# Optimization experiments

Hardware: AMD Instinct MI355X
Metric: run time of the kernel (lower is better)

Reference implementation:

```python
import jax, jax.numpy as jnp
import numpy as np

LOG_ZERO = -1e30
LOG_EPS = 1e-12


def spectral_norm(W, u0, target_radius=0.99):
    """3-step power iteration (u,v detached, as in torch no_grad) then scale W to radius 0.99."""
    Ws = jax.lax.stop_gradient(W)
    u = u0 / (jnp.linalg.norm(u0) + 1e-8)
    v = None
    for _ in range(3):
        v = Ws.T @ u
        v = v / (jnp.linalg.norm(v) + 1e-8)
        u = Ws @ v
        u = u / (jnp.linalg.norm(u) + 1e-8)
    sigma = jnp.abs(u @ (W @ v))  # grads flow through W only
    return W * (target_radius / (sigma + 1e-8))


def run_cell(x, log_h0, sign_h0, R_h, R_x, R_delta, W_delta, W_out, b, b_delta, n_groups):
    T, B, D = x.shape
    G = n_groups
    gs = D // G

    def step(carry, x_t):
        lh, sh = carry
        h_prev = sh * jnp.exp(lh)  # from_log_space
        v = x_t @ R_x.T + h_prev @ R_h.T + b
        cand = jnp.tanh(v)
        delta = jax.nn.sigmoid(x_t @ W_delta.T + h_prev @ R_delta.T + b_delta)
        h_new = (1.0 - delta) * h_prev + delta * cand
        lh_new = jnp.log(jnp.abs(h_new) + LOG_EPS)  # to_log_space
        sh_new = jnp.where(h_new >= 0, 1.0, -1.0).astype(h_new.dtype)
        compete = jax.nn.softmax(h_new.reshape(B, G, gs), axis=-1).reshape(B, D)
        out = compete * jax.nn.silu(h_new @ W_out.T)
        return (lh_new, sh_new), (out, lh_new, sh_new, h_new)

    _, (out, lh_seq, sh_seq, h_lin) = jax.lax.scan(step, (log_h0, sign_h0), x)
    log_h = jnp.concatenate([log_h0[None], lh_seq], axis=0)   # [T+1,B,D]
    sign_h = jnp.concatenate([sign_h0[None], sh_seq], axis=0)  # [T+1,B,D]
    return out, log_h, sign_h, h_lin


def setup_inputs() -> dict:
    T, B, D = 1024, 8, 1024
    key = jax.random.key(0)
    ks = jax.random.split(key, 9)
    s = 1.0 / np.sqrt(D)
    xavier = np.sqrt(2.0 / (D + D))
    return {
        "x": jax.random.normal(ks[0], (T, B, D), jnp.float32),
        "log_h0": jnp.full((B, D), LOG_ZERO, jnp.float32),
        "sign_h0": jnp.ones((B, D), jnp.float32),
        "R_h_raw": jax.random.normal(ks[1], (D, D), jnp.float32) * s,
        "R_x": jax.random.normal(ks[2], (D, D), jnp.float32) * s,
        "R_delta_raw": jax.random.normal(ks[3], (D, D), jnp.float32) * s,
        "W_delta": jax.random.normal(ks[4], (D, D), jnp.float32) * (0.1 * xavier),
        "W_out": jax.random.normal(ks[5], (D, D), jnp.float32) * xavier,
        "b": jnp.zeros((D,), jnp.float32),
        "b_delta": jnp.full((D,), -2.0, jnp.float32),
        "u_h": jax.random.normal(ks[6], (D,), jnp.float32),
        "u_delta": jax.random.normal(ks[7], (D,), jnp.float32),
        "n_groups": 32,
    }


def reference(x, log_h0, sign_h0, R_h_raw, R_x, R_delta_raw, W_delta, W_out, b, b_delta, u_h, u_delta, n_groups):
    R_h = spectral_norm(R_h_raw, u_h)
    R_delta = spectral_norm(R_delta_raw, u_delta)
    return run_cell(x, log_h0, sign_h0, R_h, R_x, R_delta, W_delta, W_out, b, b_delta, n_groups)
```

## Files before the change

kernel.cpp:

```cpp
#include <hip/hip_runtime.h>
#include <hip/hip_fp16.h>

#define DD 1024
#define TSTEPS 1024
#define BATCH 8
#define NWG 64
#define ROWS 16
#define HFS 1028

typedef _Float16 half8 __attribute__((ext_vector_type(8)));
typedef float floatx4 __attribute__((ext_vector_type(4)));

#define OUT_OFF   0
#define LOGH_OFF  8388608
#define SIGNH_OFF 16785408
#define HLIN_OFF  25182208

#define WS_SCALES  0
#define WS_SUMSQ   64
#define WS_FLAGS   128
#define WS_CNTS    384
#define WS_SPECVEC 512
#define WS_COMM    16896

__device__ __forceinline__ int aload_i(int* p) { return __hip_atomic_load(p, __ATOMIC_RELAXED, __HIP_MEMORY_SCOPE_AGENT); }
__device__ __forceinline__ float aload_f(float* p) { return __hip_atomic_load(p, __ATOMIC_RELAXED, __HIP_MEMORY_SCOPE_AGENT); }
__device__ __forceinline__ unsigned aload_u(unsigned* p) { return __hip_atomic_load(p, __ATOMIC_RELAXED, __HIP_MEMORY_SCOPE_AGENT); }
__device__ __forceinline__ void astore_f(float* p, float v) { __hip_atomic_store(p, v, __ATOMIC_RELAXED, __HIP_MEMORY_SCOPE_AGENT); }
__device__ __forceinline__ void astore_i(int* p, int v) { __hip_atomic_store(p, v, __ATOMIC_RELAXED, __HIP_MEMORY_SCOPE_AGENT); }
__device__ __forceinline__ void astore_u(unsigned* p, unsigned v) { __hip_atomic_store(p, v, __ATOMIC_RELAXED, __HIP_MEMORY_SCOPE_AGENT); }
__device__ __forceinline__ void aadd_i(int* p, int v) { (void)__hip_atomic_fetch_add(p, v, __ATOMIC_RELAXED, __HIP_MEMORY_SCOPE_AGENT); }
__device__ __forceinline__ void waitcnt_vm0() { asm volatile("s_waitcnt vmcnt(0)" ::: "memory"); }

__global__ __launch_bounds__(256) void spectral_kernel(
    const float* __restrict__ Wh, const float* __restrict__ Wd,
    const float* __restrict__ uh, const float* __restrict__ ud,
    unsigned char* __restrict__ ws) {
  const int g  = blockIdx.x >> 6;
  const int wg = blockIdx.x & 63;
  const int tid = threadIdx.x;
  const float* W  = g ? Wd : Wh;
  const float* u0 = g ? ud : uh;
  float* scales = (float*)(ws + WS_SCALES);
  float* sumsq  = (float*)(ws + WS_SUMSQ) + g*8;
  int*   cnt    = (int*)(ws + WS_CNTS) + g*8;
  float* ubuf   = (float*)(ws + WS_SPECVEC) + g*2048;
  float* vbuf   = ubuf + 1024;

  __shared__ float xs[1024];
  __shared__ float tileW[256*17];
  __shared__ float red[16*17];

  float ss = 0.f;
  for (int i2 = tid; i2 < 1024; i2 += 256) { float x = u0[i2]; ss += x*x; }
  #pragma unroll
  for (int off = 1; off < 64; off <<= 1) ss += __shfl_xor(ss, off);
  if ((tid & 63) == 0) red[tid >> 6] = ss;
  __syncthreads();
  float inv_prev = 1.f/(sqrtf(red[0]+red[1]+red[2]+red[3]) + 1e-8f);
  __syncthreads();

  for (int p = 1; p <= 6; ++p) {
    const int colmv = p & 1;
    float* dst  = colmv ? vbuf : ubuf;
    float* srcw = colmv ? ubuf : vbuf;
    float part = 0.f;
    if (colmv) {
      const int jb = wg*16;
      const int jl = tid & 15, is = tid >> 4;
      float acc = 0.f;
      for (int i0 = 0; i0 < 1024; i0 += 256) {
        __syncthreads();
        float xv = (p == 1) ? u0[i0 + tid] : aload_f(srcw + i0 + tid);
        xs[tid] = xv * inv_prev;
        const float* wr = W + (size_t)(i0 + tid)*DD + jb;
        float4 a = *(const float4*)(wr + 0);
        float4 bq = *(const float4*)(wr + 4);
        float4 cq = *(const float4*)(wr + 8);
        float4 dq = *(const float4*)(wr + 12);
        float* tr = tileW + tid*17;
        tr[0]=a.x; tr[1]=a.y; tr[2]=a.z; tr[3]=a.w;
        tr[4]=bq.x; tr[5]=bq.y; tr[6]=bq.z; tr[7]=bq.w;
        tr[8]=cq.x; tr[9]=cq.y; tr[10]=cq.z; tr[11]=cq.w;
        tr[12]=dq.x; tr[13]=dq.y; tr[14]=dq.z; tr[15]=dq.w;
        __syncthreads();
        #pragma unroll 4
        for (int ii = 0; ii < 16; ++ii)
          acc += tileW[(is*16 + ii)*17 + jl] * xs[is*16 + ii];
      }
      __syncthreads();
      red[is*17 + jl] = acc;
      __syncthreads();
      if (tid < 16) {
        float y = 0.f;
        #pragma unroll
        for (int k = 0; k < 16; ++k) y += red[k*17 + tid];
        astore_f(dst + jb + tid, y);
        part = y*y;
      }
    } else {
      const int ib = wg*16;
      for (int i2 = tid; i2 < 1024; i2 += 256) xs[i2] = aload_f(srcw + i2) * inv_prev;
      __syncthreads();
      const int r = tid >> 4, s = tid & 15;
      const float* wr = W + (size_t)(ib + r)*DD;
      float acc = 0.f;
      #pragma unroll 8
      for (int jj = 0; jj < 64; ++jj) {
        int j = s + (jj << 4);
        acc += wr[j] * xs[j];
      }
      #pragma unroll
      for (int off = 1; off < 16; off <<= 1) acc += __shfl_xor(acc, off);
      __syncthreads();
      if (s == 0) red[r] = acc;
      __syncthreads();
      if (tid < 16) {
        float y = red[tid];
        astore_f(dst + ib + tid, y);
        part = y*y;
      }
    }
    #pragma unroll
    for (int off = 1; off < 16; off <<= 1) part += __shfl_xor(part, off);
    if (tid == 0) atomicAdd(sumsq + p, part);
    waitcnt_vm0();
    __syncthreads();
    if (tid == 0) {
      aadd_i(cnt + p, 1);
      while (aload_i(cnt + p) < 64) __builtin_amdgcn_s_sleep(1);
    }
    __syncthreads();
    float stot = aload_f(sumsq + p);
    inv_prev = 1.f/(sqrtf(stot) + 1e-8f);
    __syncthreads();
  }
  if (wg == 0 && tid == 0) {
    float n2 = aload_f(sumsq + 6);
    float nn = sqrtf(n2);
    float sigma = (nn*nn)/(nn + 1e-8f);
    scales[g] = 0.99f/(sigma + 1e-8f);
  }
}

__device__ __forceinline__ half8 cvt8(const float* p) {
  float4 lo = *(const float4*)p;
  float4 hi = *(const float4*)(p+4);
  half8 h;
  h[0]=(_Float16)lo.x; h[1]=(_Float16)lo.y; h[2]=(_Float16)lo.z; h[3]=(_Float16)lo.w;
  h[4]=(_Float16)hi.x; h[5]=(_Float16)hi.y; h[6]=(_Float16)hi.z; h[7]=(_Float16)hi.w;
  return h;
}

__global__ __launch_bounds__(256) void gemm_f16(
    const float* __restrict__ A,
    const float* __restrict__ B1, const float* __restrict__ B2,
    const float* __restrict__ bias1, const float* __restrict__ bias2,
    float* __restrict__ C1, float* __restrict__ C2) {
  const int n0 = blockIdx.x * 64;
  const int m0 = blockIdx.y * 64;
  const int tid = threadIdx.x;
  const int wave = tid >> 6, lane = tid & 63;
  const int quad = lane >> 4, l16 = lane & 15;
  const bool dual = (B2 != nullptr);
  __shared__ _Float16 As[64*40];
  __shared__ _Float16 Bs1[64*40];
  __shared__ _Float16 Bs2[64*40];
  floatx4 zero = {0.f,0.f,0.f,0.f};
  floatx4 acc1[2][2] = {{zero,zero},{zero,zero}};
  floatx4 acc2[2][2] = {{zero,zero},{zero,zero}};
  const int srow = tid >> 2;
  const int sseg = (tid & 3) * 8;
  const int mb = (wave >> 1)*32, nb = (wave & 1)*32;
  for (int k0 = 0; k0 < 1024; k0 += 32) {
    __syncthreads();
    *(half8*)&As[srow*40 + sseg]  = cvt8(A  + (size_t)(m0+srow)*DD + k0 + sseg);
    *(half8*)&Bs1[srow*40 + sseg] = cvt8(B1 + (size_t)(n0+srow)*DD + k0 + sseg);
    if (dual) *(half8*)&Bs2[srow*40 + sseg] = cvt8(B2 + (size_t)(n0+srow)*DD + k0 + sseg);
    __syncthreads();
    half8 a0 = *(const half8*)&As[(mb + l16)*40 + quad*8];
    half8 a1 = *(const half8*)&As[(mb + 16 + l16)*40 + quad*8];
    half8 b0 = *(const half8*)&Bs1[(nb + l16)*40 + quad*8];
    half8 b1 = *(const half8*)&Bs1[(nb + 16 + l16)*40 + quad*8];
    acc1[0][0] = __builtin_amdgcn_mfma_f32_16x16x32_f16(a0, b0, acc1[0][0], 0,0,0);
    acc1[0][1] = __builtin_amdgcn_mfma_f32_16x16x32_f16(a0, b1, acc1[0][1], 0,0,0);
    acc1[1][0] = __builtin_amdgcn_mfma_f32_16x16x32_f16(a1, b0, acc1[1][0], 0,0,0);
    acc1[1][1] = __builtin_amdgcn_mfma_f32_16x16x32_f16(a1, b1, acc1[1][1], 0,0,0);
    if (dual) {
      half8 c0 = *(const half8*)&Bs2[(nb + l16)*40 + quad*8];
      half8 c1 = *(const half8*)&Bs2[(nb + 16 + l16)*40 + quad*8];
      acc2[0][0] = __builtin_amdgcn_mfma_f32_16x16x32_f16(a0, c0, acc2[0][0], 0,0,0);
      acc2[0][1] = __builtin_amdgcn_mfma_f32_16x16x32_f16(a0, c1, acc2[0][1], 0,0,0);
      acc2[1][0] = __builtin_amdgcn_mfma_f32_16x16x32_f16(a1, c0, acc2[1][0], 0,0,0);
      acc2[1][1] = __builtin_amdgcn_mfma_f32_16x16x32_f16(a1, c1, acc2[1][1], 0,0,0);
    }
  }
  #pragma unroll
  for (int in = 0; in < 2; ++in) {
    const int n = n0 + nb + in*16 + l16;
    const float bv1 = bias1 ? bias1[n] : 0.f;
    const float bv2 = (dual && bias2) ? bias2[n] : 0.f;
    #pragma unroll
    for (int im = 0; im < 2; ++im) {
      const int mrow = m0 + mb + im*16 + quad*4;
      floatx4 c = acc1[im][in];
      #pragma unroll
      for (int r2 = 0; r2 < 4; ++r2) C1[(size_t)(mrow + r2)*DD + n] = c[r2] + bv1;
      if (dual) {
        floatx4 c2 = acc2[im][in];
        #pragma unroll
        for (int r2 = 0; r2 < 4; ++r2) C2[(size_t)(mrow + r2)*DD + n] = c2[r2] + bv2;
      }
    }
  }
}

__global__ __launch_bounds__(256, 1) void recurrence_kernel(
    const float* __restrict__ Rh_raw, const float* __restrict__ Rd_raw,
    const float* __restrict__ logh0, const float* __restrict__ signh0,
    float* __restrict__ dout, unsigned char* __restrict__ ws) {
  const int wg = blockIdx.x;
  const int i0 = wg * ROWS;
  const int tid = threadIdx.x;
  const int wave = tid >> 6, lane = tid & 63;
  const int quad = lane >> 4, l16 = lane & 15;

  float* out_ax = dout + OUT_OFF;
  float* hlin   = dout + HLIN_OFF;
  float* logh   = dout + LOGH_OFF;
  float* signh  = dout + SIGNH_OFF;
  const float* scales = (const float*)(ws + WS_SCALES);
  unsigned* comm = (unsigned*)(ws + WS_COMM);
  int* flags = (int*)(ws + WS_FLAGS);

  __shared__ _Float16 hf[16*HFS];
  __shared__ floatx4 scr_v[4][64];
  __shared__ floatx4 scr_d[4][64];
  __shared__ unsigned hs[64];

  for (int idx = tid; idx < 8*HFS; idx += 256) hf[8*HFS + idx] = (_Float16)0.f;

  const float sh = scales[0], sd = scales[1];
  half8 afv[8], afd[8];
  {
    const float* rv = Rh_raw + (size_t)(i0 + l16)*DD;
    const float* rd = Rd_raw + (size_t)(i0 + l16)*DD;
    for (int ks = 0; ks < 8; ++ks) {
      const int kb = wave*256 + ks*32 + quad*8;
      half8 hv, hd;
      #pragma unroll
      for (int j = 0; j < 8; ++j) {
        hv[j] = (_Float16)(rv[kb + j] * sh);
        hd[j] = (_Float16)(rd[kb + j] * sd);
      }
      afv[ks] = hv; afd[ks] = hd;
    }
  }

  const int em = tid & 15;
  const int eb = tid >> 4;
  const bool ep = (tid < 128);
  const int ei = i0 + em;
  float hp = 0.f;
  if (ep) hp = signh0[eb*DD + ei] * expf(logh0[eb*DD + ei]);

  __syncthreads();

  for (int t = 0; t < TSTEPS; ++t) {
    float axv = 0.f, adv = 0.f;
    if (ep) {
      axv = out_ax[(size_t)(t*8 + eb)*DD + ei];
      adv = hlin[(size_t)(t*8 + eb)*DD + ei];
    }
    float vsum = 0.f, dsum = 0.f;
    if (t > 0) {
      {
        unsigned long long mask;
        do {
          int fv = aload_i(flags + lane);
          mask = __ballot(fv >= t);
        } while (mask != ~0ull);
      }
      {
        unsigned* src = comm + ((t-1)&1)*4096;
        unsigned rbuf[16];
        #pragma unroll
        for (int q = 0; q < 16; ++q) rbuf[q] = aload_u(src + q*256 + tid);
        #pragma unroll
        for (int q = 0; q < 16; ++q) {
          const int w = q*256 + tid;
          const int b2 = w >> 9;
          const int k2 = w & 511;
          *(unsigned*)&hf[b2*HFS + k2*2] = rbuf[q];
        }
      }
      __syncthreads();
      floatx4 av = {0.f,0.f,0.f,0.f}, ad2 = {0.f,0.f,0.f,0.f};
      const int kw = wave*256;
      #pragma unroll
      for (int ks = 0; ks < 8; ++ks) {
        half8 bfrag = *(const half8*)&hf[l16*HFS + kw + ks*32 + quad*8];
        av  = __builtin_amdgcn_mfma_f32_16x16x32_f16(afv[ks], bfrag, av,  0, 0, 0);
        ad2 = __builtin_amdgcn_mfma_f32_16x16x32_f16(afd[ks], bfrag, ad2, 0, 0, 0);
      }
      scr_v[wave][lane] = av;
      scr_d[wave][lane] = ad2;
      __syncthreads();
      if (ep) {
        const int rl = ((em >> 2) << 4) + eb;
        const int rr = em & 3;
        #pragma unroll
        for (int w2 = 0; w2 < 4; ++w2) {
          vsum += scr_v[w2][rl][rr];
          dsum += scr_d[w2][rl][rr];
        }
      }
    }
    float hn = 0.f, logv = 0.f, sgn = 1.f;
    if (ep) {
      float v  = axv + vsum;
      float dd = adv + dsum;
      float cand  = tanhf(v);
      float delta = 1.f/(1.f + expf(-dd));
      hn = (1.f - delta)*hp + delta*cand;
      hp = hn;
      logv = logf(fabsf(hn) + 1e-12f);
      sgn = (hn >= 0.f) ? 1.f : -1.f;
      ((unsigned short*)hs)[eb*16 + em] = __half_as_ushort(__float2half(hn));
    }
    __syncthreads();
    if (wave == 0) {
      const int eb2 = lane >> 3, pr = lane & 7;
      unsigned d = hs[eb2*8 + pr];
      astore_u(comm + (t&1)*4096 + eb2*512 + wg*8 + pr, d);
      waitcnt_vm0();
      if (lane == 0) astore_i(flags + wg, t + 1);
    }
    if (ep) {
      const size_t oidx = (size_t)(t*8 + eb)*DD + ei;
      hlin[oidx] = hn;
      logh[(size_t)((t+1)*8 + eb)*DD + ei] = logv;
      signh[(size_t)((t+1)*8 + eb)*DD + ei] = sgn;
    }
  }
}

__global__ __launch_bounds__(256) void out_epilogue(
    const float* __restrict__ hlin, float* __restrict__ y_out) {
  const int row = blockIdx.x;
  const int tid = threadIdx.x;
  const float* h = hlin + (size_t)row*DD;
  float* yo = y_out + (size_t)row*DD;
  const int e = tid*4;
  float4 hv = *(const float4*)(h + e);
  float4 yv = *(const float4*)(yo + e);
  float m = fmaxf(fmaxf(hv.x,hv.y), fmaxf(hv.z,hv.w));
  #pragma unroll
  for (int off = 1; off < 8; off <<= 1) m = fmaxf(m, __shfl_xor(m, off));
  float e0 = expf(hv.x - m), e1 = expf(hv.y - m), e2 = expf(hv.z - m), e3 = expf(hv.w - m);
  float s = e0+e1+e2+e3;
  #pragma unroll
  for (int off = 1; off < 8; off <<= 1) s += __shfl_xor(s, off);
  float inv = 1.f/s;
  float4 o;
  o.x = e0*inv * (yv.x/(1.f+expf(-yv.x)));
  o.y = e1*inv * (yv.y/(1.f+expf(-yv.y)));
  o.z = e2*inv * (yv.z/(1.f+expf(-yv.z)));
  o.w = e3*inv * (yv.w/(1.f+expf(-yv.w)));
  *(float4*)(yo + e) = o;
}

__global__ __launch_bounds__(256) void init_rows(
    const float* __restrict__ lh0, const float* __restrict__ sh0, float* __restrict__ dout) {
  int idx = blockIdx.x*256 + threadIdx.x;
  dout[LOGH_OFF + idx]  = lh0[idx];
  dout[SIGNH_OFF + idx] = sh0[idx];
}

extern "C" void kernel_launch(void* const* d_in, const int* in_sizes, int n_in,
                              void* d_out, int out_size, void* d_ws, size_t ws_size,
                              hipStream_t stream) {
  const float* x      = (const float*)d_in[0];
  const float* logh0  = (const float*)d_in[1];
  const float* signh0 = (const float*)d_in[2];
  const float* Rh_raw = (const float*)d_in[3];
  const float* Rx     = (const float*)d_in[4];
  const float* Rd_raw = (const float*)d_in[5];
  const float* Wdelta = (const float*)d_in[6];
  const float* Wout   = (const float*)d_in[7];
  const float* bvec   = (const float*)d_in[8];
  const float* bdelta = (const float*)d_in[9];
  const float* uh     = (const float*)d_in[10];
  const float* ud     = (const float*)d_in[11];
  float* out = (float*)d_out;
  unsigned char* ws = (unsigned char*)d_ws;

  hipMemsetAsync(ws, 0, 512, stream);
  spectral_kernel<<<128, 256, 0, stream>>>(Rh_raw, Rd_raw, uh, ud, ws);
  gemm_f16<<<dim3(16,128), 256, 0, stream>>>(x, Rx, Wdelta, bvec, bdelta,
                                             out + OUT_OFF, out + HLIN_OFF);
  init_rows<<<32, 256, 0, stream>>>(logh0, signh0, out);
  recurrence_kernel<<<NWG, 256, 0, stream>>>(Rh_raw, Rd_raw, logh0, signh0, out, ws);
  gemm_f16<<<dim3(16,128), 256, 0, stream>>>(out + HLIN_OFF, Wout, nullptr, nullptr, nullptr,
                                             out + OUT_OFF, nullptr);
  out_epilogue<<<8192, 256, 0, stream>>>(out + HLIN_OFF, out + OUT_OFF);
}
```

Before: 4.461 ms.

## Give each wave full-K row tiles in recurrent kernel, drop cross-wave reduction

Cuts the recurrent kernel from 64 to 16 workgroups of 64 rows each. Every wave now owns 16 output rows across the full K dimension and holds 32 fp16 A-fragments per matrix in registers. This removes the LDS cross-wave reduction, one __syncthreads per step and the single-wave publish step. Each wave now does its own epilogue, publishes 64-bit packed h values and sets its own flag (64 flags still polled). The cost is four times the MFMA chain length per wave, much higher register pressure, and fewer CUs sharing the serial per-step work.

```diff
diff --git a/kernel.cpp b/kernel.cpp
--- a/kernel.cpp
+++ b/kernel.cpp
@@ -4,8 +4,8 @@
 #define DD 1024
 #define TSTEPS 1024
 #define BATCH 8
-#define NWG 64
-#define ROWS 16
+#define NWG 16
+#define ROWS 64
 #define HFS 1028
 
 typedef _Float16 half8 __attribute__((ext_vector_type(8)));
@@ -28,7 +28,7 @@
 __device__ __forceinline__ unsigned aload_u(unsigned* p) { return __hip_atomic_load(p, __ATOMIC_RELAXED, __HIP_MEMORY_SCOPE_AGENT); }
 __device__ __forceinline__ void astore_f(float* p, float v) { __hip_atomic_store(p, v, __ATOMIC_RELAXED, __HIP_MEMORY_SCOPE_AGENT); }
 __device__ __forceinline__ void astore_i(int* p, int v) { __hip_atomic_store(p, v, __ATOMIC_RELAXED, __HIP_MEMORY_SCOPE_AGENT); }
-__device__ __forceinline__ void astore_u(unsigned* p, unsigned v) { __hip_atomic_store(p, v, __ATOMIC_RELAXED, __HIP_MEMORY_SCOPE_AGENT); }
+__device__ __forceinline__ void astore_u64(unsigned long long* p, unsigned long long v) { __hip_atomic_store(p, v, __ATOMIC_RELAXED, __HIP_MEMORY_SCOPE_AGENT); }
 __device__ __forceinline__ void aadd_i(int* p, int v) { (void)__hip_atomic_fetch_add(p, v, __ATOMIC_RELAXED, __HIP_MEMORY_SCOPE_AGENT); }
 __device__ __forceinline__ void waitcnt_vm0() { asm volatile("s_waitcnt vmcnt(0)" ::: "memory"); }
 
@@ -234,45 +234,56 @@
   int* flags = (int*)(ws + WS_FLAGS);
 
   __shared__ _Float16 hf[16*HFS];
-  __shared__ floatx4 scr_v[4][64];
-  __shared__ floatx4 scr_d[4][64];
-  __shared__ unsigned hs[64];
+  __shared__ float axs[512];
+  __shared__ float ads[512];
 
   for (int idx = tid; idx < 8*HFS; idx += 256) hf[8*HFS + idx] = (_Float16)0.f;
 
   const float sh = scales[0], sd = scales[1];
-  half8 afv[8], afd[8];
+  half8 afv[32], afd[32];
   {
-    const float* rv = Rh_raw + (size_t)(i0 + l16)*DD;
-    const float* rd = Rd_raw + (size_t)(i0 + l16)*DD;
-    for (int ks = 0; ks < 8; ++ks) {
-      const int kb = wave*256 + ks*32 + quad*8;
+    const float* rv = Rh_raw + (size_t)(i0 + wave*16 + l16)*DD;
+    const float* rd = Rd_raw + (size_t)(i0 + wave*16 + l16)*DD;
+    #pragma unroll
+    for (int ks = 0; ks < 32; ++ks) {
+      const int kb = ks*32 + quad*8;
+      float4 v0 = *(const float4*)(rv + kb);
+      float4 v1 = *(const float4*)(rv + kb + 4);
+      float4 d0 = *(const float4*)(rd + kb);
+      float4 d1 = *(const float4*)(rd + kb + 4);
       half8 hv, hd;
-      #pragma unroll
-      for (int j = 0; j < 8; ++j) {
-        hv[j] = (_Float16)(rv[kb + j] * sh);
-        hd[j] = (_Float16)(rd[kb + j] * sd);
-      }
+      hv[0]=(_Float16)(v0.x*sh); hv[1]=(_Float16)(v0.y*sh); hv[2]=(_Float16)(v0.z*sh); hv[3]=(_Float16)(v0.w*sh);
+      hv[4]=(_Float16)(v1.x*sh); hv[5]=(_Float16)(v1.y*sh); hv[6]=(_Float16)(v1.z*sh); hv[7]=(_Float16)(v1.w*sh);
+      hd[0]=(_Float16)(d0.x*sd); hd[1]=(_Float16)(d0.y*sd); hd[2]=(_Float16)(d0.z*sd); hd[3]=(_Float16)(d0.w*sd);
+      hd[4]=(_Float16)(d1.x*sd); hd[5]=(_Float16)(d1.y*sd); hd[6]=(_Float16)(d1.z*sd); hd[7]=(_Float16)(d1.w*sd);
       afv[ks] = hv; afd[ks] = hd;
     }
   }
 
-  const int em = tid & 15;
-  const int eb = tid >> 4;
-  const bool ep = (tid < 128);
-  const int ei = i0 + em;
-  float hp = 0.f;
-  if (ep) hp = signh0[eb*DD + ei] * expf(logh0[eb*DD + ei]);
+  const int b = l16;
+  const bool act = (l16 < 8);
+  const int r0 = wave*16 + quad*4;
+  const int ei0 = i0 + r0;
+  float hp[4] = {0.f,0.f,0.f,0.f};
+  if (act) {
+    #pragma unroll
+    for (int rr = 0; rr < 4; ++rr)
+      hp[rr] = signh0[b*DD + ei0 + rr] * expf(logh0[b*DD + ei0 + rr]);
+  }
 
   __syncthreads();
 
   for (int t = 0; t < TSTEPS; ++t) {
-    float axv = 0.f, adv = 0.f;
-    if (ep) {
-      axv = out_ax[(size_t)(t*8 + eb)*DD + ei];
-      adv = hlin[(size_t)(t*8 + eb)*DD + ei];
-    }
-    float vsum = 0.f, dsum = 0.f;
+    float ax0, ax1, ad0, ad1;
+    {
+      const int pb = tid >> 6, pr = tid & 63;
+      const size_t base = (size_t)(t*8 + pb)*DD + i0 + pr;
+      ax0 = out_ax[base];
+      ax1 = out_ax[base + 4*DD];
+      ad0 = hlin[base];
+      ad1 = hlin[base + 4*DD];
+    }
+    floatx4 av = {0.f,0.f,0.f,0.f}, ad2 = {0.f,0.f,0.f,0.f};
     if (t > 0) {
       {
         unsigned long long mask;
@@ -282,65 +293,59 @@
         } while (mask != ~0ull);
       }
       {
-        unsigned* src = comm + ((t-1)&1)*4096;
+        unsigned* src = comm + ((t-1)&1)*4096 + tid;
         unsigned rbuf[16];
         #pragma unroll
-        for (int q = 0; q < 16; ++q) rbuf[q] = aload_u(src + q*256 + tid);
+        for (int q = 0; q < 16; ++q) rbuf[q] = aload_u(src + q*256);
         #pragma unroll
         for (int q = 0; q < 16; ++q) {
           const int w = q*256 + tid;
-          const int b2 = w >> 9;
-          const int k2 = w & 511;
-          *(unsigned*)&hf[b2*HFS + k2*2] = rbuf[q];
+          *(unsigned*)&hf[(w >> 9)*HFS + (w & 511)*2] = rbuf[q];
         }
       }
-      __syncthreads();
-      floatx4 av = {0.f,0.f,0.f,0.f}, ad2 = {0.f,0.f,0.f,0.f};
-      const int kw = wave*256;
+    }
+    axs[tid] = ax0; axs[tid + 256] = ax1;
+    ads[tid] = ad0; ads[tid + 256] = ad1;
+    __syncthreads();
+    if (t > 0) {
       #pragma unroll
-      for (int ks = 0; ks < 8; ++ks) {
-        half8 bfrag = *(const half8*)&hf[l16*HFS + kw + ks*32 + quad*8];
+      for (int ks = 0; ks < 32; ++ks) {
+        half8 bfrag = *(const half8*)&hf[l16*HFS + ks*32 + quad*8];
         av  = __builtin_amdgcn_mfma_f32_16x16x32_f16(afv[ks], bfrag, av,  0, 0, 0);
         ad2 = __builtin_amdgcn_mfma_f32_16x16x32_f16(afd[ks], bfrag, ad2, 0, 0, 0);
       }
-      scr_v[wave][lane] = av;
-      scr_d[wave][lane] = ad2;
-      __syncthreads();
-      if (ep) {
-        const int rl = ((em >> 2) << 4) + eb;
-        const int rr = em & 3;
-        #pragma unroll
-        for (int w2 = 0; w2 < 4; ++w2) {
-          vsum += scr_v[w2][rl][rr];
-          dsum += scr_d[w2][rl][rr];
-        }
-      }
-    }
-    float hn = 0.f, logv = 0.f, sgn = 1.f;
-    if (ep) {
-      float v  = axv + vsum;
-      float dd = adv + dsum;
-      float cand  = tanhf(v);
-      float delta = 1.f/(1.f + expf(-dd));
-      hn = (1.f - delta)*hp + delta*cand;
-      hp = hn;
-      logv = logf(fabsf(hn) + 1e-12f);
-      sgn = (hn >= 0.f) ? 1.f : -1.f;
-      ((unsigned short*)hs)[eb*16 + em] = __half_as_ushort(__float2half(hn));
-    }
-    __syncthreads();
-    if (wave == 0) {
-      const int eb2 = lane >> 3, pr = lane & 7;
-      unsigned d = hs[eb2*8 + pr];
-      astore_u(comm + (t&1)*4096 + eb2*512 + wg*8 + pr, d);
-      waitcnt_vm0();
-      if (lane == 0) astore_i(flags + wg, t + 1);
-    }
-    if (ep) {
-      const size_t oidx = (size_t)(t*8 + eb)*DD + ei;
-      hlin[oidx] = hn;
-      logh[(size_t)((t+1)*8 + eb)*DD + ei] = logv;
-      signh[(size_t)((t+1)*8 + eb)*DD + ei] = sgn;
+    }
+    float h4[4];
+    if (act) {
+      #pragma unroll
+      for (int rr = 0; rr < 4; ++rr) {
+        float v  = axs[b*64 + r0 + rr] + av[rr];
+        float dd = ads[b*64 + r0 + rr] + ad2[rr];
+        float cand  = tanhf(v);
+        float delta = 1.f/(1.f + expf(-dd));
+        float hn = (1.f - delta)*hp[rr] + delta*cand;
+        hp[rr] = hn; h4[rr] = hn;
+      }
+      unsigned d0 = (unsigned)__half_as_ushort(__float2half(h4[0])) |
+                    ((unsigned)__half_as_ushort(__float2half(h4[1])) << 16);
+      unsigned d1 = (unsigned)__half_as_ushort(__float2half(h4[2])) |
+                    ((unsigned)__half_as_ushort(__float2half(h4[3])) << 16);
+      unsigned long long pl = ((unsigned long long)d1 << 32) | (unsigned long long)d0;
+      astore_u64((unsigned long long*)(comm + (t&1)*4096 + b*512 + (ei0 >> 1)), pl);
+    }
+    waitcnt_vm0();
+    if (lane == 0) astore_i(flags + (wg<<2) + wave, t + 1);
+    if (act) {
+      const size_t ob = (size_t)(t*8 + b)*DD + ei0;
+      *(float4*)&hlin[ob] = *(float4*)h4;
+      float4 lg, sg;
+      lg.x = logf(fabsf(h4[0]) + 1e-12f); sg.x = (h4[0] >= 0.f) ? 1.f : -1.f;
+      lg.y = logf(fabsf(h4[1]) + 1e-12f); sg.y = (h4[1] >= 0.f) ? 1.f : -1.f;
+      lg.z = logf(fabsf(h4[2]) + 1e-12f); sg.z = (h4[2] >= 0.f) ? 1.f : -1.f;
+      lg.w = logf(fabsf(h4[3]) + 1e-12f); sg.w = (h4[3] >= 0.f) ? 1.f : -1.f;
+      const size_t ob2 = (size_t)((t+1)*8 + b)*DD + ei0;
+      *(float4*)&logh[ob2] = lg;
+      *(float4*)&signh[ob2] = sg;
     }
   }
 }
```

After: 4.637 ms. +3.9%, slower.
